# Kernel optimization log

Measured on AMD Instinct MI355X. Metric: run time of the kernel, lower is better.

## Reference

```python
import jax, jax.numpy as jnp
import numpy as np
import math

BS, S, D = 2, 2048, 2048
DOWN, UP, H, RD = 512, 1024, 16, 32
HD = D // H            # 128, used only in softmax scale
VD = UP // H           # 64 per-head value dim
CD = UP // H           # 64 per-head content q/k dim
SCALE = math.sqrt(HD) + math.sqrt(RD)


def _rope(x, head_dim):
    # x: [bs, heads, seq, head_dim]; standard rotate-half RoPE
    seq = x.shape[2]
    inv_freq = 1.0 / (10000.0 ** (jnp.arange(0, head_dim, 2, dtype=jnp.float32) / head_dim))
    freqs = jnp.arange(seq, dtype=jnp.float32)[:, None] * inv_freq[None, :]  # [S, hd/2]
    emb = jnp.concatenate([freqs, freqs], axis=-1)                            # [S, hd]
    cos = jnp.cos(emb)[None, None]
    sin = jnp.sin(emb)[None, None]
    x1, x2 = x[..., : head_dim // 2], x[..., head_dim // 2 :]
    rot = jnp.concatenate([-x2, x1], axis=-1)
    return x * cos + rot * sin


def setup_inputs() -> dict:
    key = jax.random.key(0)
    ks = jax.random.split(key, 10)
    sd = 0.02
    inp = {
        'h': jax.random.normal(ks[0], (BS, S, D), jnp.float32),
        'mask': jnp.tril(jnp.ones((1, 1, S, S), jnp.int32)),
        'Wdkv': jax.random.normal(ks[1], (DOWN, D), jnp.float32) * sd,
        'bdkv': jnp.zeros((DOWN,), jnp.float32),
        'Wuk': jax.random.normal(ks[2], (UP, DOWN), jnp.float32) * sd,
        'buk': jnp.zeros((UP,), jnp.float32),
        'Wuv': jax.random.normal(ks[3], (UP, DOWN), jnp.float32) * sd,
        'buv': jnp.zeros((UP,), jnp.float32),
        'Wdq': jax.random.normal(ks[4], (DOWN, D), jnp.float32) * sd,
        'bdq': jnp.zeros((DOWN,), jnp.float32),
        'Wuq': jax.random.normal(ks[5], (UP, DOWN), jnp.float32) * sd,
        'buq': jnp.zeros((UP,), jnp.float32),
        'Wqr': jax.random.normal(ks[6], (RD * H, DOWN), jnp.float32) * sd,
        'bqr': jnp.zeros((RD * H,), jnp.float32),
        'Wkr': jax.random.normal(ks[7], (RD, D), jnp.float32) * sd,
        'bkr': jnp.zeros((RD,), jnp.float32),
        'Wfc': jax.random.normal(ks[8], (D, H * VD), jnp.float32) * sd,
        'bfc': jnp.zeros((D,), jnp.float32),
    }
    return inp


def reference(h, mask, Wdkv, bdkv, Wuk, buk, Wuv, buv, Wdq, bdq, Wuq, buq,
              Wqr, bqr, Wkr, bkr, Wfc, bfc):
    bs, seq, _ = h.shape
    # low-rank KV path
    c_kv = h @ Wdkv.T + bdkv                                   # [bs,S,DOWN]
    k_c = (c_kv @ Wuk.T + buk).reshape(bs, seq, H, CD).transpose(0, 2, 1, 3)
    v_c = (c_kv @ Wuv.T + buv).reshape(bs, seq, H, VD).transpose(0, 2, 1, 3)
    # low-rank Q path
    c_q = h @ Wdq.T + bdq                                      # [bs,S,DOWN]
    q_c = (c_q @ Wuq.T + buq).reshape(bs, seq, H, CD).transpose(0, 2, 1, 3)
    # decoupled RoPE paths
    q_r = _rope((c_q @ Wqr.T + bqr).reshape(bs, seq, H, RD).transpose(0, 2, 1, 3), RD)
    k_r = _rope((h @ Wkr.T + bkr).reshape(bs, seq, 1, RD).transpose(0, 2, 1, 3), RD)
    k_r = jnp.broadcast_to(k_r, (bs, H, seq, RD))              # shared RoPE key across heads
    q = jnp.concatenate([q_c, q_r], axis=-1)                   # [bs,H,S,CD+RD]
    k = jnp.concatenate([k_c, k_r], axis=-1)
    scores = jnp.einsum('bhqd,bhkd->bhqk', q, k)
    # NB: original applies mask BEFORE dividing by scale
    scores = jnp.where(mask == 0, -1e9, scores)
    probs = jax.nn.softmax(scores / SCALE, axis=-1)
    out = jnp.einsum('bhqk,bhkd->bhqd', probs, v_c)            # [bs,H,S,VD]
    out = out.transpose(0, 2, 1, 3).reshape(bs, seq, H * VD)
    return out @ Wfc.T + bfc
```

## Files before the change

kernel.cpp:

```cpp
#include <hip/hip_runtime.h>
#include <hip/hip_bf16.h>
#include <math.h>

typedef unsigned short u16;
typedef __attribute__((ext_vector_type(8))) short bf16x8;
typedef __attribute__((ext_vector_type(4))) float f32x4;
typedef __attribute__((ext_vector_type(16))) float f32x16;

namespace {

constexpr int BS = 2;
constexpr int S = 2048;
constexpr int D = 2048;
constexpr int DOWN = 512;
constexpr int UP = 1024;
constexpr int H = 16;
constexpr int RD = 32;
constexpr int VD = 64;
constexpr int QKD = 96;
constexpr int M = BS * S;
constexpr int N1 = 1152;
constexpr int N2 = 2048;
constexpr int N3 = 1536;
constexpr long ROPE_V8 = (long)BS * H * S * 4;

__device__ __forceinline__ float b2f(u16 u) {
  unsigned int x = ((unsigned int)u) << 16;
  return __uint_as_float(x);
}
__device__ __forceinline__ u16 f2b(float f) {
  unsigned int u = __float_as_uint(f);
  u += 0x7fff + ((u >> 16) & 1);
  return (u16)(u >> 16);
}
__device__ __forceinline__ void store_out(float* p, float v) { *p = v; }
__device__ __forceinline__ void store_out(u16* p, float v) { *p = f2b(v); }

__device__ __forceinline__ void async16(const u16* g, u16* lds) {
  __builtin_amdgcn_global_load_lds(
      (const __attribute__((address_space(1))) unsigned int*)g,
      (__attribute__((address_space(3))) unsigned int*)lds, 16, 0, 0);
}

__device__ __forceinline__ float exp2_fast(float x) {
#if __has_builtin(__builtin_amdgcn_exp2f)
  return __builtin_amdgcn_exp2f(x);
#else
  float r;
  asm("v_exp_f32 %0, %1" : "=v"(r) : "v"(x));
  return r;
#endif
}

__device__ __forceinline__ unsigned pkbf(float a, float b) {
  union { __hip_bfloat162 h; unsigned u; } c;
  c.h = __float22bfloat162_rn(make_float2(a, b));
  return c.u;
}
__device__ __forceinline__ void plswap(unsigned& a, unsigned& b) {
  asm("v_permlane32_swap_b32 %0, %1" : "+v"(a), "+v"(b));
}

__device__ __forceinline__ f32x4 mfma32(bf16x8 a, bf16x8 b, f32x4 c) {
  return __builtin_amdgcn_mfma_f32_16x16x32_bf16(a, b, c, 0, 0, 0);
}
__device__ __forceinline__ f32x16 mfma3216(bf16x8 a, bf16x8 b, f32x16 c) {
  return __builtin_amdgcn_mfma_f32_32x32x16_bf16(a, b, c, 0, 0, 0);
}

__global__ __launch_bounds__(256) void prep_kernel(
    const float* __restrict__ h, const float* __restrict__ Wdkv,
    const float* __restrict__ Wdq, const float* __restrict__ Wkr,
    const float* __restrict__ Wuk, const float* __restrict__ Wuv,
    const float* __restrict__ Wuq, const float* __restrict__ Wqr,
    const float* __restrict__ Wfc, const float* __restrict__ bdkv,
    const float* __restrict__ bdq, const float* __restrict__ bkr,
    const float* __restrict__ buk, const float* __restrict__ buv,
    const float* __restrict__ buq, const float* __restrict__ bqr,
    u16* __restrict__ hb, u16* __restrict__ Wcat1, u16* __restrict__ Wcat2,
    u16* __restrict__ Wcat3, u16* __restrict__ Wfcb,
    float* __restrict__ bcat1, float* __restrict__ bcat2,
    float* __restrict__ bcat3, float* __restrict__ ct, float* __restrict__ st) {
  const long i = (long)blockIdx.x * 256 + threadIdx.x;
  if (i >= 3630240) return;
  const float SC = 1.44269504088896f / (sqrtf(128.f) + sqrtf(32.f));
  if (i < 3620864) {
    const float* src; u16* dst; long off; float scl = 1.f;
    if      (i < 2097152) { src = h;    dst = hb;              off = i; }
    else if (i < 2359296) { src = Wdkv; dst = Wcat1;           off = i - 2097152; }
    else if (i < 2621440) { src = Wdq;  dst = Wcat1 + 1048576; off = i - 2359296; }
    else if (i < 2637824) { src = Wkr;  dst = Wcat1 + 2097152; off = i - 2621440; }
    else if (i < 2768896) { src = Wuk;  dst = Wcat2;           off = i - 2637824; }
    else if (i < 2899968) { src = Wuv;  dst = Wcat2 + 524288;  off = i - 2768896; }
    else if (i < 3031040) { src = Wuq;  dst = Wcat3;           off = i - 2899968; scl = SC; }
    else if (i < 3096576) { src = Wqr;  dst = Wcat3 + 524288;  off = i - 3031040; scl = SC; }
    else                  { src = Wfc;  dst = Wfcb;            off = i - 3096576; }
    float4 v = ((const float4*)src)[off];
    ushort4 o;
    o.x = f2b(v.x * scl); o.y = f2b(v.y * scl);
    o.z = f2b(v.z * scl); o.w = f2b(v.w * scl);
    ((ushort4*)dst)[off] = o;
  } else if (i < 3622048) {
    long j0 = (i - 3620864) * 4;
#pragma unroll
    for (int e = 0; e < 4; ++e) {
      long j = j0 + e;
      if (j < N1) {
        float v = 0.f;
        if (j < 512) v = bdkv[j];
        else if (j < 1024) v = bdq[j - 512];
        else if (j < 1056) v = bkr[j - 1024];
        bcat1[j] = v;
      } else if (j < N1 + N2) {
        long jj = j - N1;
        bcat2[jj] = (jj < 1024) ? buk[jj] : buv[jj - 1024];
      } else {
        long jj = j - N1 - N2;
        bcat3[jj] = ((jj < 1024) ? buq[jj] : bqr[jj - 1024]) * SC;
      }
    }
  } else {
    long k0 = (i - 3622048) * 4;
#pragma unroll
    for (int e = 0; e < 4; ++e) {
      long k = k0 + e;
      int s = (int)(k >> 4), r = (int)(k & 15);
      float f = powf(10000.f, -(float)r / 16.f);
      float th = (float)s * f;
      ct[k] = cosf(th);
      st[k] = sinf(th);
    }
  }
}

template <int BM, int BN, typename OutT>
__device__ __forceinline__ void gemm_body_sb(
    const u16* __restrict__ A, int lda, const u16* __restrict__ W, int ldw,
    const float* __restrict__ bias, OutT* __restrict__ C, int ldc, int K,
    int m0, int n0) {
  constexpr int MW = BM / 32;
  constexpr int NW = BN / 32;
  constexpr int AI = BM / 16;
  constexpr int TI = AI + BN / 16;
  __shared__ u16 As[BM * 32];
  __shared__ u16 Bs[BN * 32];
  const int t = threadIdx.x;
  const int lane = t & 63, wave = t >> 6;
  const int wm = (wave >> 1) * (BM / 2), wn = (wave & 1) * (BN / 2);
  const int lrow = lane & 15, lk = (lane >> 4) * 8;
  const int srow = lane >> 2, scol = (lane & 3) * 8;
  f32x4 acc[MW][NW] = {};
  for (int k0 = 0; k0 < K; k0 += 32) {
    __syncthreads();
    for (int i = wave; i < TI; i += 4) {
      if (i < AI) {
        int r = i * 16 + srow;
        async16(A + (size_t)(m0 + r) * lda + k0 + scol, As + i * 512);
      } else {
        int r = (i - AI) * 16 + srow;
        async16(W + (size_t)(n0 + r) * ldw + k0 + scol, Bs + (i - AI) * 512);
      }
    }
    __syncthreads();
    bf16x8 af[MW], bfr[NW];
#pragma unroll
    for (int i = 0; i < MW; ++i)
      af[i] = *(const bf16x8*)(As + (wm + i * 16 + lrow) * 32 + lk);
#pragma unroll
    for (int i = 0; i < NW; ++i)
      bfr[i] = *(const bf16x8*)(Bs + (wn + i * 16 + lrow) * 32 + lk);
#pragma unroll
    for (int mi = 0; mi < MW; ++mi)
#pragma unroll
      for (int ni = 0; ni < NW; ++ni)
        acc[mi][ni] = mfma32(af[mi], bfr[ni], acc[mi][ni]);
  }
#pragma unroll
  for (int mi = 0; mi < MW; ++mi)
#pragma unroll
    for (int ni = 0; ni < NW; ++ni)
#pragma unroll
      for (int r = 0; r < 4; ++r) {
        int m = m0 + wm + mi * 16 + (lane >> 4) * 4 + r;
        int n = n0 + wn + ni * 16 + lrow;
        store_out(C + (size_t)m * ldc + n, acc[mi][ni][r] + bias[n]);
      }
}

template <int BM, int BN, typename F>
__device__ __forceinline__ void gemm_core_db(
    const u16* __restrict__ A, int lda, const u16* __restrict__ W, int ldw,
    const float* __restrict__ bias, int K, int m0, int n0, F&& emit) {
  constexpr int MW = BM / 32;
  constexpr int NW = BN / 32;
  constexpr int AI = BM / 16;
  constexpr int TI = AI + BN / 16;
  __shared__ u16 As[2][BM * 32];
  __shared__ u16 Bs[2][BN * 32];
  const int t = threadIdx.x;
  const int lane = t & 63, wave = t >> 6;
  const int wm = (wave >> 1) * (BM / 2), wn = (wave & 1) * (BN / 2);
  const int lrow = lane & 15, lk = (lane >> 4) * 8;
  const int srow = lane >> 2, scol = (lane & 3) * 8;
  f32x4 acc[MW][NW] = {};

  auto stage = [&](int buf, int k0) {
    for (int i = wave; i < TI; i += 4) {
      if (i < AI) {
        int r = i * 16 + srow;
        async16(A + (size_t)(m0 + r) * lda + k0 + scol, &As[buf][i * 512]);
      } else {
        int r = (i - AI) * 16 + srow;
        async16(W + (size_t)(n0 + r) * ldw + k0 + scol,
                &Bs[buf][(i - AI) * 512]);
      }
    }
  };

  const int nt = K / 32;
  stage(0, 0);
  __syncthreads();
  for (int ti = 0; ti < nt; ++ti) {
    const int buf = ti & 1;
    if (ti + 1 < nt) stage(buf ^ 1, (ti + 1) * 32);
    bf16x8 af[MW], bfr[NW];
#pragma unroll
    for (int i = 0; i < MW; ++i)
      af[i] = *(const bf16x8*)(&As[buf][(wm + i * 16 + lrow) * 32 + lk]);
#pragma unroll
    for (int i = 0; i < NW; ++i)
      bfr[i] = *(const bf16x8*)(&Bs[buf][(wn + i * 16 + lrow) * 32 + lk]);
#pragma unroll
    for (int mi = 0; mi < MW; ++mi)
#pragma unroll
      for (int ni = 0; ni < NW; ++ni)
        acc[mi][ni] = mfma32(af[mi], bfr[ni], acc[mi][ni]);
    __syncthreads();
  }
#pragma unroll
  for (int mi = 0; mi < MW; ++mi)
#pragma unroll
    for (int ni = 0; ni < NW; ++ni)
#pragma unroll
      for (int r = 0; r < 4; ++r) {
        int m = m0 + wm + mi * 16 + (lane >> 4) * 4 + r;
        int n = n0 + wn + ni * 16 + lrow;
        emit(m, n, acc[mi][ni][r] + bias[n]);
      }
}

template <int BM, int BN, typename OutT>
__global__ __launch_bounds__(256) void gemm_bt_sb(
    const u16* __restrict__ A, int lda, const u16* __restrict__ W, int ldw,
    const float* __restrict__ bias, OutT* __restrict__ C, int ldc, int K) {
  gemm_body_sb<BM, BN, OutT>(A, lda, W, ldw, bias, C, ldc, K,
                             blockIdx.x * BM, blockIdx.y * BN);
}

template <int BM, int BN, typename OutT>
__global__ __launch_bounds__(256) void gemm_bt_db(
    const u16* __restrict__ A, int lda, const u16* __restrict__ W, int ldw,
    const float* __restrict__ bias, OutT* __restrict__ C, int ldc, int K) {
  gemm_core_db<BM, BN>(A, lda, W, ldw, bias, K, blockIdx.x * BM,
                       blockIdx.y * BN, [&](int m, int n, float v) {
                         store_out(C + (size_t)m * ldc + n, v);
                       });
}

__global__ __launch_bounds__(256) void gemm_up_fused(
    const u16* __restrict__ C1v, const u16* __restrict__ Wcat2,
    const u16* __restrict__ Wcat3, const float* __restrict__ bcat2,
    const float* __restrict__ bcat3, u16* __restrict__ C2,
    u16* __restrict__ C3, u16* __restrict__ Qp, u16* __restrict__ Kp) {
  const int by = blockIdx.y;
  if (by < 16) {
    gemm_core_db<128, 128>(
        C1v, N1, Wcat2, DOWN, bcat2, DOWN, blockIdx.x * 128, by * 128,
        [&](int m, int n, float v) {
          if (n < 1024) {
            int b = m >> 11, s = m & 2047, hh = n >> 6, d = n & 63;
            Kp[((size_t)(b * 16 + hh) * 2048 + s) * 96 + d] = f2b(v);
          } else {
            C2[(size_t)m * N2 + n] = f2b(v);
          }
        });
  } else {
    gemm_core_db<128, 128>(
        C1v + DOWN, N1, Wcat3, DOWN, bcat3, DOWN, blockIdx.x * 128,
        (by - 16) * 128, [&](int m, int n, float v) {
          if (n < 1024) {
            int b = m >> 11, s = m & 2047, hh = n >> 6, d = n & 63;
            Qp[((size_t)(b * 16 + hh) * 2048 + s) * 96 + d] = f2b(v);
          } else {
            C3[(size_t)m * N3 + n] = f2b(v);
          }
        });
  }
}

__global__ __launch_bounds__(256) void reshape_kernel(
    const u16* __restrict__ qr,
    const u16* __restrict__ kr,
    const float* __restrict__ ct, const float* __restrict__ st,
    const u16* __restrict__ vin,
    u16* __restrict__ Qp, u16* __restrict__ Kp, u16* __restrict__ VtB) {
  const int bid = blockIdx.x;
  if (bid < 2048) {
    const long i = (long)bid * 256 + threadIdx.x;
    const int which = (i >= ROPE_V8);
    const long j = which ? i - ROPE_V8 : i;
    const int gg = (int)(j & 3);
    const long row = j >> 2;
    const int s = (int)(row & (S - 1));
    const int h = (int)((row >> 11) & 15);
    const int b = (int)(row >> 15);
    const int r0 = gg * 8;
    const float* cb = ct + s * 16 + (r0 & 15);
    const float* sn = st + s * 16 + (r0 & 15);
    const float sg = (r0 < 16) ? -1.f : 1.f;
    bf16x8 o;
    if (which == 0) {
      const u16* qrow = qr + (size_t)(b * S + s) * N3 + h * RD;
      bf16x8 x8 = *(const bf16x8*)(qrow + r0);
      bf16x8 xp8 = *(const bf16x8*)(qrow + (r0 ^ 16));
#pragma unroll
      for (int e = 0; e < 8; ++e) {
        float val = b2f((u16)x8[e]) * cb[e] + sg * b2f((u16)xp8[e]) * sn[e];
        o[e] = (short)f2b(val);
      }
      *(bf16x8*)(Qp + row * 96 + 64 + r0) = o;
    } else {
      const u16* krow = kr + (size_t)(b * S + s) * N1;
      bf16x8 x8 = *(const bf16x8*)(krow + r0);
      bf16x8 xp8 = *(const bf16x8*)(krow + (r0 ^ 16));
#pragma unroll
      for (int e = 0; e < 8; ++e) {
        float val = b2f((u16)x8[e]) * cb[e] + sg * b2f((u16)xp8[e]) * sn[e];
        o[e] = (short)f2b(val);
      }
      *(bf16x8*)(Kp + row * 96 + 64 + r0) = o;
    }
  } else {
    __shared__ u16 tile[64][72];
    const int tb = bid - 2048;
    const int m0 = (tb & 63) * 64;
    const int h = tb >> 6;
    const int r = threadIdx.x >> 2, c0 = (threadIdx.x & 3) * 16;
    *(bf16x8*)(&tile[r][c0]) =
        *(const bf16x8*)(vin + (size_t)(m0 + r) * N2 + h * VD + c0);
    *(bf16x8*)(&tile[r][c0 + 8]) =
        *(const bf16x8*)(vin + (size_t)(m0 + r) * N2 + h * VD + c0 + 8);
    __syncthreads();
    bf16x8 o0, o1;
#pragma unroll
    for (int jj = 0; jj < 8; ++jj) {
      o0[jj] = (short)tile[c0 + jj][r];
      o1[jj] = (short)tile[c0 + 8 + jj][r];
    }
    const int b = m0 / S, sb = m0 % S;
    size_t dst = ((size_t)(b * H + h) * 64 + ((sb + c0) >> 5)) * 2048 +
                 (size_t)r * 32 + ((sb + c0) & 31);
    *(bf16x8*)(VtB + dst) = o0;
    *(bf16x8*)(VtB + dst + 8) = o1;
  }
}

__global__ __launch_bounds__(256, 3) void attn_mfma(
    const u16* __restrict__ Qp, const u16* __restrict__ Kp,
    const u16* __restrict__ Vt, u16* __restrict__ attnb) {
  const int t = threadIdx.x, wave = t >> 6, lane = t & 63;
  const int l31 = lane & 31, hw = lane >> 5;
  const int xcd = (int)(blockIdx.x & 7), sub = (int)(blockIdx.x >> 3);
  const int bh = xcd * 4 + (sub & 3);
  const int tile = 63 - (sub >> 2);
  const int b = bh >> 4, h = bh & 15;
  const int q0w = tile * 32;
  const size_t hbo = (size_t)bh * S;
  constexpr long KSTR = (long)4 * 32 * QKD;
  constexpr long VSTR = (long)4 * 2048;

  __shared__ float red[3][64][33];

  bf16x8 qf[6];
  {
    const u16* qrow = Qp + (hbo + q0w + l31) * QKD + hw * 8;
#pragma unroll
    for (int c = 0; c < 6; ++c) qf[c] = *(const bf16x8*)(qrow + c * 16);
  }
  const f32x16 ZERO16 = {0,0,0,0,0,0,0,0,0,0,0,0,0,0,0,0};
  f32x16 O0 = ZERO16, O1 = ZERO16;
  float lsum = 0.f;
  const int q_abs = q0w + l31;
  const u16* vptr = Vt + (size_t)bh * 64 * 2048 + l31 * 32 + 8 * hw +
                    (size_t)wave * 2048;
  const u16* kptr = Kp + (hbo + (size_t)(wave * 32 + l31)) * QKD + hw * 8;

  auto loadK = [&](bf16x8* kf) {
#pragma unroll
    for (int c = 0; c < 6; ++c) kf[c] = *(const bf16x8*)(kptr + c * 16);
  };
  auto loadV = [&](const u16* p, bf16x8* vf) {
    vf[0] = *(const bf16x8*)(p);
    vf[1] = *(const bf16x8*)(p + 16);
    vf[2] = *(const bf16x8*)(p + 1024);
    vf[3] = *(const bf16x8*)(p + 1040);
  };
  auto finish = [&](const f32x16& sa, const f32x16& sb, const bf16x8* vf,
                    int m) {
    float e[16];
    if (m == tile) {
      const int k0 = m * 32;
#pragma unroll
      for (int r = 0; r < 16; ++r) {
        int key_abs = k0 + (r & 3) + 8 * (r >> 2) + 4 * hw;
        float v = exp2_fast(sa[r] + sb[r]);
        e[r] = (key_abs <= q_abs) ? v : 0.f;
      }
    } else {
#pragma unroll
      for (int r = 0; r < 16; ++r) e[r] = exp2_fast(sa[r] + sb[r]);
    }
    {
      float p0 = (e[0] + e[1]) + (e[2] + e[3]);
      float p1 = (e[4] + e[5]) + (e[6] + e[7]);
      float p2 = (e[8] + e[9]) + (e[10] + e[11]);
      float p3 = (e[12] + e[13]) + (e[14] + e[15]);
      lsum += (p0 + p1) + (p2 + p3);
    }
    unsigned w0 = pkbf(e[0], e[1]),   w1 = pkbf(e[2], e[3]);
    unsigned w2 = pkbf(e[4], e[5]),   w3 = pkbf(e[6], e[7]);
    unsigned w4 = pkbf(e[8], e[9]),   w5 = pkbf(e[10], e[11]);
    unsigned w6 = pkbf(e[12], e[13]), w7 = pkbf(e[14], e[15]);
    plswap(w0, w2); plswap(w1, w3); plswap(w4, w6); plswap(w5, w7);
    union { unsigned u[4]; bf16x8 v; } ua, ub;
    ua.u[0] = w0; ua.u[1] = w1; ua.u[2] = w2; ua.u[3] = w3;
    ub.u[0] = w4; ub.u[1] = w5; ub.u[2] = w6; ub.u[3] = w7;
    __builtin_amdgcn_s_setprio(1);
    O0 = mfma3216(ua.v, vf[0], O0);
    O1 = mfma3216(ua.v, vf[2], O1);
    O0 = mfma3216(ub.v, vf[1], O0);
    O1 = mfma3216(ub.v, vf[3], O1);
    __builtin_amdgcn_s_setprio(0);
  };

  if (tile >= wave) {
    bf16x8 kf[6], vfE[4], vfO[4];
    loadK(kf);
    loadV(vptr, vfE);
    int m = wave;
    while (true) {
      {
        const bool pf = (m + 4 <= tile);
        if (pf) { vptr += VSTR; loadV(vptr, vfO); }
        __builtin_amdgcn_s_setprio(1);
        f32x16 sa = mfma3216(kf[0], qf[0], ZERO16);
        f32x16 sb = mfma3216(kf[1], qf[1], ZERO16);
        sa = mfma3216(kf[2], qf[2], sa);
        sb = mfma3216(kf[3], qf[3], sb);
        sa = mfma3216(kf[4], qf[4], sa);
        sb = mfma3216(kf[5], qf[5], sb);
        __builtin_amdgcn_s_setprio(0);
        if (pf) { kptr += KSTR; loadK(kf); }
        finish(sa, sb, vfE, m);
      }
      m += 4;
      if (m > tile) break;
      {
        const bool pf = (m + 4 <= tile);
        if (pf) { vptr += VSTR; loadV(vptr, vfE); }
        __builtin_amdgcn_s_setprio(1);
        f32x16 sa = mfma3216(kf[0], qf[0], ZERO16);
        f32x16 sb = mfma3216(kf[1], qf[1], ZERO16);
        sa = mfma3216(kf[2], qf[2], sa);
        sb = mfma3216(kf[3], qf[3], sb);
        sa = mfma3216(kf[4], qf[4], sa);
        sb = mfma3216(kf[5], qf[5], sb);
        __builtin_amdgcn_s_setprio(0);
        if (pf) { kptr += KSTR; loadK(kf); }
        finish(sa, sb, vfO, m);
      }
      m += 4;
      if (m > tile) break;
    }
  }

  if (wave > 0) {
#pragma unroll
    for (int r = 0; r < 16; ++r) {
      red[wave - 1][lane][r] = O0[r];
      red[wave - 1][lane][16 + r] = O1[r];
    }
    red[wave - 1][lane][32] = lsum;
  }
  __syncthreads();
  if (wave == 0) {
#pragma unroll
    for (int w = 0; w < 3; ++w) {
#pragma unroll
      for (int r = 0; r < 16; ++r) {
        O0[r] += red[w][lane][r];
        O1[r] += red[w][lane][16 + r];
      }
      lsum += red[w][lane][32];
    }
    float tot = lsum + __shfl_xor(lsum, 32);
    u16* ob = attnb + (size_t)b * S * UP + h * VD;
#pragma unroll
    for (int r = 0; r < 16; ++r) {
      int rowq = (r & 3) + 8 * (r >> 2) + 4 * hw;
      float linv = 1.f / __shfl(tot, rowq);
      size_t rowoff = (size_t)(q0w + rowq) * UP;
      ob[rowoff + l31] = f2b(O0[r] * linv);
      ob[rowoff + 32 + l31] = f2b(O1[r] * linv);
    }
  }
}

}

extern "C" void kernel_launch(void* const* d_in, const int* in_sizes, int n_in,
                              void* d_out, int out_size, void* d_ws, size_t ws_size,
                              hipStream_t stream) {
  const float* h    = (const float*)d_in[0];
  const float* Wdkv = (const float*)d_in[2];
  const float* bdkv = (const float*)d_in[3];
  const float* Wuk  = (const float*)d_in[4];
  const float* buk  = (const float*)d_in[5];
  const float* Wuv  = (const float*)d_in[6];
  const float* buv  = (const float*)d_in[7];
  const float* Wdq  = (const float*)d_in[8];
  const float* bdq  = (const float*)d_in[9];
  const float* Wuq  = (const float*)d_in[10];
  const float* buq  = (const float*)d_in[11];
  const float* Wqr  = (const float*)d_in[12];
  const float* bqr  = (const float*)d_in[13];
  const float* Wkr  = (const float*)d_in[14];
  const float* bkr  = (const float*)d_in[15];
  const float* Wfc  = (const float*)d_in[16];
  const float* bfc  = (const float*)d_in[17];
  float* out = (float*)d_out;

  u16* p = (u16*)d_ws;
  u16* hb    = p; p += (size_t)M * D;
  u16* Wcat1 = p; p += (size_t)N1 * D;
  u16* Wcat2 = p; p += (size_t)N2 * DOWN;
  u16* Wcat3 = p; p += (size_t)N3 * DOWN;
  u16* Wfcb  = p; p += (size_t)D * UP;
  u16* C1    = p; p += (size_t)M * N1;
  u16* C2    = p; p += (size_t)M * N2;
  u16* C3    = p; p += (size_t)M * N3;
  u16* Qp    = p; p += 6291456;
  u16* Kp    = p; p += 6291456;
  u16* Vt    = p; p += (size_t)UP * M;
  float* bcat1 = (float*)p; p += 2 * N1;
  float* bcat2 = (float*)p; p += 2 * N2;
  float* bcat3 = (float*)p; p += 2 * N3;
  float* ct = (float*)p; p += 2 * S * 16;
  float* st = (float*)p; p += 2 * S * 16;
  u16* attnb = C1;

  prep_kernel<<<dim3(14181), 256, 0, stream>>>(
      h, Wdkv, Wdq, Wkr, Wuk, Wuv, Wuq, Wqr, Wfc,
      bdkv, bdq, bkr, buk, buv, buq, bqr,
      hb, Wcat1, Wcat2, Wcat3, Wfcb, bcat1, bcat2, bcat3, ct, st);

  gemm_bt_sb<64, 64, u16><<<dim3(M / 64, N1 / 64), 256, 0, stream>>>(
      hb, D, Wcat1, D, bcat1, C1, N1, D);
  gemm_up_fused<<<dim3(M / 128, 28), 256, 0, stream>>>(
      C1, Wcat2, Wcat3, bcat2, bcat3, C2, C3, Qp, Kp);

  reshape_kernel<<<dim3(3072), 256, 0, stream>>>(
      C3 + UP, C1 + 2 * DOWN, ct, st, C2 + UP, Qp, Kp, Vt);

  attn_mfma<<<dim3(2048), 256, 0, stream>>>(Qp, Kp, Vt, attnb);

  gemm_bt_db<64, 128, float><<<dim3(M / 64, D / 128), 256, 0, stream>>>(
      attnb, UP, Wfcb, UP, bfc, out, D, UP);
}
```

Baseline: 306.4 us.

## Triple-buffer GEMM LDS staging with vmcnt-based waits instead of syncthreads

Replaces the single-buffered and double-buffered GEMM cores with one three-stage pipeline that prefetches two K-tiles ahead into LDS. Each iteration waits with an explicit s_waitcnt vmcnt(LW) plus a raw s_barrier, so loads for the newest tile can stay in flight. All three GEMM launches (down-projection, fused up-projection, output projection) now use this path. The cost is 1.5x the LDS of the double-buffered version, which may lower occupancy, and correctness relies on the hand-counted per-wave load count matching the vmcnt values.

```diff
diff --git a/kernel.cpp b/kernel.cpp
--- a/kernel.cpp
+++ b/kernel.cpp
@@ -40,6 +40,15 @@
   __builtin_amdgcn_global_load_lds(
       (const __attribute__((address_space(1))) unsigned int*)g,
       (__attribute__((address_space(3))) unsigned int*)lds, 16, 0, 0);
+}
+
+template <int N>
+__device__ __forceinline__ void waitcnt_vm() {
+  if constexpr (N == 0) asm volatile("s_waitcnt vmcnt(0)" ::: "memory");
+  else if constexpr (N == 2) asm volatile("s_waitcnt vmcnt(2)" ::: "memory");
+  else if constexpr (N == 3) asm volatile("s_waitcnt vmcnt(3)" ::: "memory");
+  else if constexpr (N == 4) asm volatile("s_waitcnt vmcnt(4)" ::: "memory");
+  else static_assert(N == 0, "unsupported vmcnt");
 }
 
 __device__ __forceinline__ float exp2_fast(float x) {
@@ -133,70 +142,17 @@
   }
 }
 
-template <int BM, int BN, typename OutT>
-__device__ __forceinline__ void gemm_body_sb(
-    const u16* __restrict__ A, int lda, const u16* __restrict__ W, int ldw,
-    const float* __restrict__ bias, OutT* __restrict__ C, int ldc, int K,
-    int m0, int n0) {
-  constexpr int MW = BM / 32;
-  constexpr int NW = BN / 32;
-  constexpr int AI = BM / 16;
-  constexpr int TI = AI + BN / 16;
-  __shared__ u16 As[BM * 32];
-  __shared__ u16 Bs[BN * 32];
-  const int t = threadIdx.x;
-  const int lane = t & 63, wave = t >> 6;
-  const int wm = (wave >> 1) * (BM / 2), wn = (wave & 1) * (BN / 2);
-  const int lrow = lane & 15, lk = (lane >> 4) * 8;
-  const int srow = lane >> 2, scol = (lane & 3) * 8;
-  f32x4 acc[MW][NW] = {};
-  for (int k0 = 0; k0 < K; k0 += 32) {
-    __syncthreads();
-    for (int i = wave; i < TI; i += 4) {
-      if (i < AI) {
-        int r = i * 16 + srow;
-        async16(A + (size_t)(m0 + r) * lda + k0 + scol, As + i * 512);
-      } else {
-        int r = (i - AI) * 16 + srow;
-        async16(W + (size_t)(n0 + r) * ldw + k0 + scol, Bs + (i - AI) * 512);
-      }
-    }
-    __syncthreads();
-    bf16x8 af[MW], bfr[NW];
-#pragma unroll
-    for (int i = 0; i < MW; ++i)
-      af[i] = *(const bf16x8*)(As + (wm + i * 16 + lrow) * 32 + lk);
-#pragma unroll
-    for (int i = 0; i < NW; ++i)
-      bfr[i] = *(const bf16x8*)(Bs + (wn + i * 16 + lrow) * 32 + lk);
-#pragma unroll
-    for (int mi = 0; mi < MW; ++mi)
-#pragma unroll
-      for (int ni = 0; ni < NW; ++ni)
-        acc[mi][ni] = mfma32(af[mi], bfr[ni], acc[mi][ni]);
-  }
-#pragma unroll
-  for (int mi = 0; mi < MW; ++mi)
-#pragma unroll
-    for (int ni = 0; ni < NW; ++ni)
-#pragma unroll
-      for (int r = 0; r < 4; ++r) {
-        int m = m0 + wm + mi * 16 + (lane >> 4) * 4 + r;
-        int n = n0 + wn + ni * 16 + lrow;
-        store_out(C + (size_t)m * ldc + n, acc[mi][ni][r] + bias[n]);
-      }
-}
-
 template <int BM, int BN, typename F>
-__device__ __forceinline__ void gemm_core_db(
+__device__ __forceinline__ void gemm_core_pipe(
     const u16* __restrict__ A, int lda, const u16* __restrict__ W, int ldw,
     const float* __restrict__ bias, int K, int m0, int n0, F&& emit) {
   constexpr int MW = BM / 32;
   constexpr int NW = BN / 32;
   constexpr int AI = BM / 16;
   constexpr int TI = AI + BN / 16;
-  __shared__ u16 As[2][BM * 32];
-  __shared__ u16 Bs[2][BN * 32];
+  constexpr int LW = TI / 4;
+  __shared__ u16 As[3][BM * 32];
+  __shared__ u16 Bs[3][BN * 32];
   const int t = threadIdx.x;
   const int lane = t & 63, wave = t >> 6;
   const int wm = (wave >> 1) * (BM / 2), wn = (wave & 1) * (BN / 2);
@@ -219,10 +175,12 @@
 
   const int nt = K / 32;
   stage(0, 0);
-  __syncthreads();
+  stage(1, 32);
+  waitcnt_vm<LW>();
+  __builtin_amdgcn_s_barrier();
   for (int ti = 0; ti < nt; ++ti) {
-    const int buf = ti & 1;
-    if (ti + 1 < nt) stage(buf ^ 1, (ti + 1) * 32);
+    const int buf = ti % 3;
+    if (ti + 2 < nt) stage((ti + 2) % 3, (ti + 2) * 32);
     bf16x8 af[MW], bfr[NW];
 #pragma unroll
     for (int i = 0; i < MW; ++i)
@@ -235,7 +193,11 @@
 #pragma unroll
       for (int ni = 0; ni < NW; ++ni)
         acc[mi][ni] = mfma32(af[mi], bfr[ni], acc[mi][ni]);
-    __syncthreads();
+    if (ti + 1 < nt) {
+      if (ti + 2 < nt) waitcnt_vm<LW>();
+      else waitcnt_vm<0>();
+      __builtin_amdgcn_s_barrier();
+    }
   }
 #pragma unroll
   for (int mi = 0; mi < MW; ++mi)
@@ -250,21 +212,13 @@
 }
 
 template <int BM, int BN, typename OutT>
-__global__ __launch_bounds__(256) void gemm_bt_sb(
+__global__ __launch_bounds__(256) void gemm_bt_pipe(
     const u16* __restrict__ A, int lda, const u16* __restrict__ W, int ldw,
     const float* __restrict__ bias, OutT* __restrict__ C, int ldc, int K) {
-  gemm_body_sb<BM, BN, OutT>(A, lda, W, ldw, bias, C, ldc, K,
-                             blockIdx.x * BM, blockIdx.y * BN);
-}
-
-template <int BM, int BN, typename OutT>
-__global__ __launch_bounds__(256) void gemm_bt_db(
-    const u16* __restrict__ A, int lda, const u16* __restrict__ W, int ldw,
-    const float* __restrict__ bias, OutT* __restrict__ C, int ldc, int K) {
-  gemm_core_db<BM, BN>(A, lda, W, ldw, bias, K, blockIdx.x * BM,
-                       blockIdx.y * BN, [&](int m, int n, float v) {
-                         store_out(C + (size_t)m * ldc + n, v);
-                       });
+  gemm_core_pipe<BM, BN>(A, lda, W, ldw, bias, K, blockIdx.x * BM,
+                         blockIdx.y * BN, [&](int m, int n, float v) {
+                           store_out(C + (size_t)m * ldc + n, v);
+                         });
 }
 
 __global__ __launch_bounds__(256) void gemm_up_fused(
@@ -274,7 +228,7 @@
     u16* __restrict__ C3, u16* __restrict__ Qp, u16* __restrict__ Kp) {
   const int by = blockIdx.y;
   if (by < 16) {
-    gemm_core_db<128, 128>(
+    gemm_core_pipe<128, 128>(
         C1v, N1, Wcat2, DOWN, bcat2, DOWN, blockIdx.x * 128, by * 128,
         [&](int m, int n, float v) {
           if (n < 1024) {
@@ -285,7 +239,7 @@
           }
         });
   } else {
-    gemm_core_db<128, 128>(
+    gemm_core_pipe<128, 128>(
         C1v + DOWN, N1, Wcat3, DOWN, bcat3, DOWN, blockIdx.x * 128,
         (by - 16) * 128, [&](int m, int n, float v) {
           if (n < 1024) {
@@ -564,7 +518,7 @@
       bdkv, bdq, bkr, buk, buv, buq, bqr,
       hb, Wcat1, Wcat2, Wcat3, Wfcb, bcat1, bcat2, bcat3, ct, st);
 
-  gemm_bt_sb<64, 64, u16><<<dim3(M / 64, N1 / 64), 256, 0, stream>>>(
+  gemm_bt_pipe<64, 64, u16><<<dim3(M / 64, N1 / 64), 256, 0, stream>>>(
       hb, D, Wcat1, D, bcat1, C1, N1, D);
   gemm_up_fused<<<dim3(M / 128, 28), 256, 0, stream>>>(
       C1, Wcat2, Wcat3, bcat2, bcat3, C2, C3, Qp, Kp);
@@ -574,6 +528,6 @@
 
   attn_mfma<<<dim3(2048), 256, 0, stream>>>(Qp, Kp, Vt, attnb);
 
-  gemm_bt_db<64, 128, float><<<dim3(M / 64, D / 128), 256, 0, stream>>>(
+  gemm_bt_pipe<64, 128, float><<<dim3(M / 64, D / 128), 256, 0, stream>>>(
       attnb, UP, Wfcb, UP, bfc, out, D, UP);
 }
```

Measured after the change: 340.2 us. +11.0%, slower.
